# Kernel tuning notes

Measured on AMD Instinct MI355X. Metric: run time of the kernel, lower is better.

The kernel has to match this reference:

```python
import jax, jax.numpy as jnp
import numpy as np

CUTOFF = 4.0
D_RBF = 20


def _rbf_consts():
    # e3nn soft_one_hot_linspace, basis='gaussian', cutoff=False
    values = np.linspace(0.0, CUTOFF, D_RBF)
    step = values[1] - values[0]
    # RadialBasis normalization buffers: 4000 uniform samples, unbiased std
    rs = np.linspace(0.0, CUTOFF, 4001)[1:]
    bs = np.exp(-(((rs[:, None] - values[None, :]) / step) ** 2)) / 1.12
    mean = bs.mean(0)
    inv_std = 1.0 / bs.std(0, ddof=1)
    return (jnp.asarray(values, jnp.float32), jnp.float32(step),
            jnp.asarray(mean, jnp.float32), jnp.asarray(inv_std, jnp.float32))


def setup_inputs() -> dict:
    N, P, E = 2000, 50000, 300000
    Ds, Dv, H, HO = 256, 128, 256, 128
    din = Ds + Dv + D_RBF + Dv  # 532
    key = jax.random.key(0)
    ks = jax.random.split(key, 12)
    atom_xyz = jax.random.uniform(ks[0], (N, 3), jnp.float32, 0.0, 8.0)
    probe_xyz = jax.random.uniform(ks[1], (P, 3), jnp.float32, 0.0, 8.0)
    cell = jnp.eye(3, dtype=jnp.float32)[None] * 8.0  # [1,3,3]
    src = jax.random.randint(ks[2], (E,), 0, N)
    dst = jax.random.randint(ks[3], (E,), 0, P)
    edges = jnp.stack([src, dst], axis=-1).astype(jnp.int32)  # [E,2]
    edges_displacement = jax.random.randint(ks[4], (E, 3), -1, 2).astype(jnp.float32)
    S_final = jax.random.normal(ks[5], (N, Ds), jnp.float32)
    V_final = jax.random.normal(ks[6], (N, Dv, 3), jnp.float32)
    s = 0.02
    return {
        'atom_xyz': atom_xyz, 'probe_xyz': probe_xyz, 'cell': cell,
        'edges': edges, 'edges_displacement': edges_displacement,
        'S_final': S_final, 'V_final': V_final,
        'ln_gamma': jnp.ones((din,), jnp.float32),
        'ln_beta': jnp.zeros((din,), jnp.float32),
        'W1': jax.random.normal(ks[7], (din, H), jnp.float32) * s,
        'b1': jnp.zeros((H,), jnp.float32),
        'W2': jax.random.normal(ks[8], (H, H), jnp.float32) * s,
        'b2': jnp.zeros((H,), jnp.float32),
        'Wo1': jax.random.normal(ks[9], (H, HO), jnp.float32) * s,
        'bo1': jnp.zeros((HO,), jnp.float32),
        'Wo2': jax.random.normal(ks[10], (HO, 1), jnp.float32) * s,
        'bo2': jnp.full((1,), -10.0, jnp.float32),
    }


def reference(atom_xyz, probe_xyz, cell, edges, edges_displacement,
              S_final, V_final, ln_gamma, ln_beta,
              W1, b1, W2, b2, Wo1, bo1, Wo2, bo2):
    values, step, rbf_mean, rbf_inv_std = _rbf_consts()
    src, dst = edges[:, 0], edges[:, 1]
    # PBC displacement: edges_displacement @ cell (single graph -> cell[0])
    disp = edges_displacement @ cell[0]                     # [E,3]
    vec = probe_xyz[dst] - (atom_xyz[src] + disp)           # [E,3]
    d = jnp.maximum(jnp.linalg.norm(vec, axis=-1, keepdims=True), 1e-8)
    r_hat = vec / d                                         # [E,3]
    ds = d[:, 0]                                            # [E]
    # RBF (gaussian soft one-hot) + normalization
    diff = (ds[:, None] - values) / step
    e = (jnp.exp(-diff * diff) / 1.12 - rbf_mean) * rbf_inv_std  # [E,20]
    x = ds / CUTOFF
    x5 = x ** 5
    env = (1.0 - 21.0 * x5 + 35.0 * x5 * x - 15.0 * x5 * x * x)
    env = env * (ds < CUTOFF).astype(jnp.float32)           # [E]
    # geometric invariants
    q = jnp.einsum('ek,eck->ec', r_hat, V_final[src])       # [E,Dv]
    n_atom = jnp.linalg.norm(V_final, axis=-1)              # [N,Dv]
    feat = jnp.concatenate([S_final[src], n_atom[src], e, q], axis=-1)  # [E,532]
    # LayerNorm
    mu = feat.mean(-1, keepdims=True)
    var = feat.var(-1, keepdims=True)
    feat = (feat - mu) * jax.lax.rsqrt(var + 1e-5) * ln_gamma + ln_beta
    # message MLP
    h = jax.nn.silu(feat @ W1 + b1)
    h = jax.nn.silu(h @ W2 + b2)                            # [E,256]
    # envelope-weighted scatter-add to probes
    m_p = jax.ops.segment_sum(h * env[:, None], dst,
                              num_segments=probe_xyz.shape[0])  # [P,256]
    # output MLP
    o = jax.nn.silu(m_p @ Wo1 + bo1)
    rho = o @ Wo2 + bo2                                     # [P,1]
    return rho[:, 0]
```

## Files before the change

### kernel.cpp

```cpp
#include <hip/hip_runtime.h>
#include <hip/hip_bf16.h>
#include <hip/hip_fp16.h>

#define DIN 532
#define DRBF 20
#define EB 32

typedef __attribute__((ext_vector_type(8))) short s8v;
typedef __attribute__((ext_vector_type(4))) float f4v;

static __device__ __forceinline__ float silu_f(float x){
    return x * __builtin_amdgcn_rcpf(1.0f + __expf(-x));
}
static __device__ __forceinline__ short f2bf(float x){
    __hip_bfloat16 b = __float2bfloat16(x);
    return *(short*)&b;
}
static __device__ __forceinline__ s8v pack8(float4 f0, float4 f1){
    s8v r;
    r[0]=f2bf(f0.x); r[1]=f2bf(f0.y); r[2]=f2bf(f0.z); r[3]=f2bf(f0.w);
    r[4]=f2bf(f1.x); r[5]=f2bf(f1.y); r[6]=f2bf(f1.z); r[7]=f2bf(f1.w);
    return r;
}
static __device__ __forceinline__ s8v pack8p(const float* p){
    float4 f0 = *(const float4*)p, f1 = *(const float4*)(p + 4);
    return pack8(f0, f1);
}
static __device__ __forceinline__ bool detect_bf16(const void* cellraw){
    float c0 = ((const float*)cellraw)[0];
    return !(c0 > 7.5f && c0 < 8.5f);
}
static __device__ __forceinline__ float loadr(const void* p, bool isbf, long idx){
    if (isbf) return __bfloat162float(((const __hip_bfloat16*)p)[idx]);
    return ((const float*)p)[idx];
}

struct ConvArgs {
    const void* src[10];
    float*      dst[10];
    int         sz[10];
    int         total;
};

__global__ __launch_bounds__(256) void k_pre(ConvArgs ca,
    const void* W1r, const void* gammar, const void* betar, const void* b1r,
    const void* W2r, const void* Wo1r, const void* cellraw,
    float* Gpart, float* Bpart, float* rbfc,
    short* w1ef, short* w2f, short* w1f, short* wo1f)
{
    int b = blockIdx.x, t = threadIdx.x;
    bool isbf = detect_bf16(cellraw);
    if (b < 256){
        int stride = 256 * 256;
        for (int i = b*256 + t; i < ca.total; i += stride){
            int idx = i, k = 0;
            while (idx >= ca.sz[k]) { idx -= ca.sz[k]; k++; }
            float v = 0.0f;
            if (ca.src[k]) v = loadr(ca.src[k], isbf, idx);
            ca.dst[k][idx] = v;
        }
        return;
    }
    int pb = b - 256;
    if (pb < 17){
        int i0 = pb * 32, i1 = min(i0 + 32, DIN);
        float g = 0.0f, bb = 0.0f;
        for (int i = i0; i < i1; i++){
            float w  = loadr(W1r, isbf, (long)i*256 + t);
            g  += loadr(gammar, isbf, i) * w;
            bb += loadr(betar,  isbf, i) * w;
        }
        if (pb == 0) bb += loadr(b1r, isbf, t);
        Gpart[pb*256 + t] = g;
        Bpart[pb*256 + t] = bb;
        return;
    }
    if (pb == 17){
        __shared__ float ssum[DRBF][8], ssq[DRBF][8];
        if (t < 160){
            int m = t >> 3, c = t & 7;
            const float step = 4.0f/19.0f;
            float vm = step * m;
            float s = 0.0f, ss = 0.0f;
            for (int i = c*500 + 1; i <= c*500 + 500; i++){
                float r = 0.001f * (float)i;
                float u = (r - vm) / step;
                float bv = __expf(-u*u) * (1.0f/1.12f);
                s += bv; ss += bv*bv;
            }
            ssum[m][c] = s; ssq[m][c] = ss;
        }
        __syncthreads();
        if (t < DRBF){
            float s = 0.0f, ss = 0.0f;
            for (int c = 0; c < 8; c++){ s += ssum[t][c]; ss += ssq[t][c]; }
            float mean = s / 4000.0f;
            float var  = (ss - s*s/4000.0f) / 3999.0f;
            rbfc[t]        = mean;
            rbfc[DRBF + t] = rsqrtf(var);
        }
        return;
    }
    int wid = t >> 6, lane = t & 63;
    int q8 = (lane >> 4) * 8, nl = lane & 15;
    if (pb <= 21){
        int f = (pb - 18)*4 + wid;
        for (int j = 0; j < 8; j++){
            int kk = q8 + j;
            int n  = f*16 + nl;
            float v = (kk < DRBF)
                ? loadr(gammar, isbf, 384 + kk) * loadr(W1r, isbf, (long)(384 + kk)*256 + n)
                : 0.0f;
            w1ef[((f << 6) | lane)*8 + j] = f2bf(v);
        }
    } else if (pb <= 53){
        int f = (pb - 22)*4 + wid;
        int ks = f & 7;
        for (int j = 0; j < 8; j++){
            int kk = ks*32 + q8 + j;
            int n  = (f >> 3)*16 + nl;
            w2f[((f << 6) | lane)*8 + j] = f2bf(loadr(W2r, isbf, (long)kk*256 + n));
        }
    } else if (pb <= 117){
        int f = (pb - 54)*4 + wid;
        int ksg = f >> 4, ntg = f & 15;
        int base;
        if (ksg < 8)       base = ksg * 32;
        else if (ksg < 12) base = 256 + (ksg - 8) * 32;
        else               base = 404 + (ksg - 12) * 32;
        for (int j = 0; j < 8; j++){
            int kk = base + q8 + j;
            int n  = ntg*16 + nl;
            w1f[((f << 6) | lane)*8 + j] =
                f2bf(loadr(gammar, isbf, kk) * loadr(W1r, isbf, (long)kk*256 + n));
        }
    } else {
        int f = (pb - 118)*4 + wid;
        int ks = f & 7;
        for (int j = 0; j < 8; j++){
            int kk = ks*32 + q8 + j;
            int n  = (f >> 3)*16 + nl;
            wo1f[((f << 6) | lane)*8 + j] = f2bf(loadr(Wo1r, isbf, (long)kk*128 + n));
        }
    }
}

__global__ __launch_bounds__(1024) void k_mid(
    const float* S, const float* V, const short* w1f, float4* AM,
    float* scal, int N,
    const int* edges, const void* edraw, const float* cell,
    const float* axyz, const float* pxyz,
    int* etot, int* flag, int2* esd, float4* geo, float* m_p,
    const void* cellraw, int E,
    const float* Gpart, const float* Bpart, float* Gv, float* Bb,
    int GA, int GG)
{
    int b = blockIdx.x, t = threadIdx.x;
    int wid = t >> 6, lane = t & 63;

    if (b < GA){
        __shared__ float Sl[16][260];
        __shared__ float Vxl[16][132], Vyl[16][132], Vzl[16][132], nll[16][132];
        int q = lane >> 4, ml = lane & 15;
        int a0 = b * 16;

        #pragma unroll
        for (int rep = 0; rep < 4; rep++){
            int i = rep*1024 + t;
            int a = i >> 8, c = i & 255;
            Sl[a][c] = S[(size_t)min(a0 + a, N - 1)*256 + c];
        }
        #pragma unroll
        for (int rep = 0; rep < 2; rep++){
            int i = rep*1024 + t;
            int a = i >> 7, c = i & 127;
            const float* vp = &V[(size_t)min(a0 + a, N - 1)*384 + 3*c];
            float x = vp[0], y = vp[1], z = vp[2];
            Vxl[a][c] = x; Vyl[a][c] = y; Vzl[a][c] = z;
            nll[a][c] = sqrtf(x*x + y*y + z*z);
        }
        __syncthreads();

        {
            float v[11];
            #pragma unroll
            for (int k = 0; k < 11; k++) v[k] = 0.0f;
            #pragma unroll
            for (int e0 = 0; e0 < 256; e0 += 64){
                float s = Sl[wid][e0 + lane];
                v[0] += s; v[1] += s*s;
            }
            #pragma unroll
            for (int e0 = 0; e0 < 128; e0 += 64){
                int e = e0 + lane;
                float n = nll[wid][e], x = Vxl[wid][e], y = Vyl[wid][e], z = Vzl[wid][e];
                v[0] += n;   v[1] += n*n;
                v[2] += x;   v[3] += y;   v[4] += z;
                v[5] += x*x; v[6] += x*y; v[7] += x*z;
                v[8] += y*y; v[9] += y*z; v[10] += z*z;
            }
            #pragma unroll
            for (int k = 0; k < 11; k++)
                for (int off2 = 32; off2 > 0; off2 >>= 1)
                    v[k] += __shfl_xor(v[k], off2, 64);
            if (lane == 0 && a0 + wid < N)
                for (int k = 0; k < 11; k++) scal[(a0 + wid)*12 + k] = v[k];
        }

        f4v zz = {0.0f, 0.0f, 0.0f, 0.0f};
        f4v aA1 = zz, aM0 = zz, aM1 = zz, aM2 = zz;

        #pragma unroll
        for (int ks = 0; ks < 8; ks++){
            s8v av = pack8p(&Sl[ml][ks*32 + q*8]);
            s8v bf = ((const s8v*)w1f)[(((ks << 4) | wid) << 6) | lane];
            aA1 = __builtin_amdgcn_mfma_f32_16x16x32_bf16(av, bf, aA1, 0, 0, 0);
        }
        #pragma unroll
        for (int ks = 0; ks < 4; ks++){
            s8v av = pack8p(&nll[ml][ks*32 + q*8]);
            s8v bf = ((const s8v*)w1f)[((((8 + ks) << 4) | wid) << 6) | lane];
            aA1 = __builtin_amdgcn_mfma_f32_16x16x32_bf16(av, bf, aA1, 0, 0, 0);
        }
        #pragma unroll
        for (int ks = 0; ks < 4; ks++){
            s8v ax = pack8p(&Vxl[ml][ks*32 + q*8]);
            s8v ay = pack8p(&Vyl[ml][ks*32 + q*8]);
            s8v az = pack8p(&Vzl[ml][ks*32 + q*8]);
            s8v bf = ((const s8v*)w1f)[((((12 + ks) << 4) | wid) << 6) | lane];
            aM0 = __builtin_amdgcn_mfma_f32_16x16x32_bf16(ax, bf, aM0, 0, 0, 0);
            aM1 = __builtin_amdgcn_mfma_f32_16x16x32_bf16(ay, bf, aM1, 0, 0, 0);
            aM2 = __builtin_amdgcn_mfma_f32_16x16x32_bf16(az, bf, aM2, 0, 0, 0);
        }

        #pragma unroll
        for (int reg = 0; reg < 4; reg++){
            int atom = a0 + (q << 2) + reg;
            if (atom < N)
                AM[(size_t)atom*256 + ((wid << 4) | ml)] =
                    make_float4(aA1[reg], aM0[reg], aM1[reg], aM2[reg]);
        }
        return;
    }

    if (b < GA + GG){
        __shared__ int wcnt[16], wbase[16];
        bool isbf = detect_bf16(cellraw);
        float c0=cell[0],c1=cell[1],c2=cell[2],c3=cell[3],c4=cell[4];
        float c5=cell[5],c6=cell[6],c7=cell[7],c8=cell[8];
        int i = (b - GA)*1024 + t;

        bool act = false;
        int s = 0, dd = 0;
        float r0 = 0.f, r1 = 0.f, r2 = 0.f, dn = 0.f;
        if (i < E){
            s = edges[2*i]; dd = edges[2*i + 1];
            float d0 = loadr(edraw, isbf, 3L*i);
            float d1 = loadr(edraw, isbf, 3L*i + 1);
            float d2 = loadr(edraw, isbf, 3L*i + 2);
            float dx = d0*c0 + d1*c3 + d2*c6;
            float dy = d0*c1 + d1*c4 + d2*c7;
            float dz = d0*c2 + d1*c5 + d2*c8;
            float vx = pxyz[3*dd]   - (axyz[3*s]   + dx);
            float vy = pxyz[3*dd+1] - (axyz[3*s+1] + dy);
            float vz = pxyz[3*dd+2] - (axyz[3*s+2] + dz);
            dn = fmaxf(sqrtf(vx*vx + vy*vy + vz*vz), 1e-8f);
            act = dn < 4.0f;
            float inv = __builtin_amdgcn_rcpf(dn);
            r0 = vx*inv; r1 = vy*inv; r2 = vz*inv;
        }
        unsigned long long mask = __ballot(act);
        if (lane == 0) wcnt[wid] = __popcll(mask);
        __syncthreads();
        if (t == 0){
            int tot = 0;
            #pragma unroll
            for (int w2 = 0; w2 < 16; w2++) tot += wcnt[w2];
            int base = tot ? atomicAdd(etot, tot) : 0;
            int run = base;
            #pragma unroll
            for (int w2 = 0; w2 < 16; w2++){ wbase[w2] = run; run += wcnt[w2]; }
        }
        __syncthreads();
        if (act){
            int pos = wbase[wid] + __popcll(mask & ((1ULL << lane) - 1ULL));
            esd[pos] = make_int2(s, dd);
            geo[pos] = make_float4(r0, r1, r2, dn);
            if (atomicExch(&flag[dd], 1) == 0){
                float4 z = make_float4(0.f, 0.f, 0.f, 0.f);
                float4* p = (float4*)&m_p[(size_t)dd*256];
                #pragma unroll 4
                for (int k = 0; k < 64; k++) p[k] = z;
            }
        }
        return;
    }

    if (t < 256){
        float g = 0.0f, bb = 0.0f;
        #pragma unroll
        for (int i = 0; i < 17; i++){
            g  += Gpart[i*256 + t];
            bb += Bpart[i*256 + t];
        }
        Gv[t] = g;
        Bb[t] = bb;
    }
}

__global__ __launch_bounds__(256, 2) void k_edge(
    const int2* esd, const float4* geo, const int* etot, const float* scal,
    const float4* AM, const float* Gv, const float* Bb, const float* b2,
    const short* w1ef, const short* w2f, const float* rbfc, float* m_p)
{
    __shared__ float Gl[256], Bbl[256], b2l[256];
    __shared__ float rmean[DRBF], rinv[DRBF];
    __shared__ int   esrc[EB], edst[EB];
    __shared__ float rh0[EB], rh1[EB], rh2[EB], envv[EB], muv[EB], av[EB];
    __shared__ __align__(16) short ebfl[EB][32];
    __shared__ __align__(16) short afrag[2][8][64][8];

    int t = threadIdx.x, wid = t >> 6, lane = t & 63;
    int q = lane >> 4, ml_ = lane & 15;
    Gl[t] = Gv[t]; Bbl[t] = Bb[t]; b2l[t] = b2[t];
    if (t < DRBF){ rmean[t] = rbfc[t]; rinv[t] = rbfc[DRBF + t]; }
    __syncthreads();

    int Ea = etot[0];
    int ntiles = (Ea + EB - 1) / EB;

    for (int tile = blockIdx.x; tile < ntiles; tile += gridDim.x){
        if (t < EB){
            int epos = tile*EB + t;
            if (epos < Ea){
                int2 sd = esd[epos];
                float4 g = geo[epos];
                float r0 = g.x, r1 = g.y, r2 = g.z, dn = g.w;
                float x = dn * 0.25f;
                float x2 = x*x, x4 = x2*x2, x5 = x4*x;
                float env = 1.0f - 21.0f*x5 + 35.0f*x5*x - 15.0f*x5*x2;
                const float step = 4.0f/19.0f;
                float se = 0.0f, sse = 0.0f;
                for (int m = 0; m < DRBF; m++){
                    float u  = (dn - step*m) / step;
                    float bv = __expf(-u*u) * (1.0f/1.12f);
                    float em = (bv - rmean[m]) * rinv[m];
                    ebfl[t][m] = f2bf(em);
                    se += em; sse += em*em;
                }
                for (int m = DRBF; m < 32; m++) ebfl[t][m] = 0;
                const float* sc = &scal[sd.x*12];
                float sumq = r0*sc[2] + r1*sc[3] + r2*sc[4];
                float ssqq = r0*r0*sc[5] + r1*r1*sc[8] + r2*r2*sc[10]
                           + 2.0f*(r0*r1*sc[6] + r0*r2*sc[7] + r1*r2*sc[9]);
                float mu  = (sc[0] + se + sumq) * (1.0f/(float)DIN);
                float msq = (sc[1] + sse + ssqq) * (1.0f/(float)DIN);
                float a   = rsqrtf(fmaxf(msq - mu*mu, 0.0f) + 1e-5f);
                esrc[t] = sd.x; edst[t] = sd.y;
                rh0[t] = r0; rh1[t] = r1; rh2[t] = r2;
                envv[t] = env; muv[t] = mu; av[t] = a;
            } else {
                esrc[t] = 0; edst[t] = 0;
                rh0[t] = rh1[t] = rh2[t] = 0.0f;
                envv[t] = 0.0f; muv[t] = 0.0f; av[t] = 0.0f;
                for (int m = 0; m < 32; m++) ebfl[t][m] = 0;
            }
        }
        __syncthreads();

        f4v zz = {0.0f, 0.0f, 0.0f, 0.0f};
        f4v az[2][4];
        s8v ea0 = *(const s8v*)&ebfl[ml_][q*8];
        s8v ea1 = *(const s8v*)&ebfl[16 + ml_][q*8];
        #pragma unroll
        for (int nt = 0; nt < 4; nt++){
            s8v bw = ((const s8v*)w1ef)[(((wid << 2) | nt) << 6) | lane];
            az[0][nt] = __builtin_amdgcn_mfma_f32_16x16x32_bf16(ea0, bw, zz, 0, 0, 0);
            az[1][nt] = __builtin_amdgcn_mfma_f32_16x16x32_bf16(ea1, bw, zz, 0, 0, 0);
        }

        float gk[4], bbk[4];
        #pragma unroll
        for (int nt = 0; nt < 4; nt++){
            int k = (wid << 6) | (nt << 4) | ml_;
            gk[nt] = Gl[k]; bbk[nt] = Bbl[k];
        }
        #pragma unroll
        for (int mt = 0; mt < 2; mt++){
            #pragma unroll
            for (int reg = 0; reg < 4; reg++){
                int e_ = (mt << 4) | (q << 2) | reg;
                int s_ = esrc[e_];
                float r0 = rh0[e_], r1 = rh1[e_], r2 = rh2[e_];
                float mu = muv[e_], a_ = av[e_];
                const float4* AMr = &AM[(size_t)s_*256 + ((wid << 6) | ml_)];
                #pragma unroll
                for (int nt = 0; nt < 4; nt++){
                    float4 am = AMr[nt << 4];
                    float z = az[mt][nt][reg] + am.x + r0*am.y + r1*am.z + r2*am.w;
                    float y = a_*(z - mu*gk[nt]) + bbk[nt];
                    float h1 = silu_f(y);
                    int ks = (wid << 1) | (nt >> 1);
                    int col = ((nt & 1) << 4) | ml_;
                    int lanep = ((col >> 3) << 4) | (q << 2) | reg;
                    afrag[mt][ks][lanep][col & 7] = f2bf(h1);
                }
            }
        }
        __syncthreads();

        f4v acc[2][4];
        #pragma unroll
        for (int mt = 0; mt < 2; mt++)
            #pragma unroll
            for (int nt = 0; nt < 4; nt++) acc[mt][nt] = zz;
        #pragma unroll
        for (int ks = 0; ks < 8; ks++){
            s8v a0 = *(const s8v*)&afrag[0][ks][lane][0];
            s8v a1 = *(const s8v*)&afrag[1][ks][lane][0];
            #pragma unroll
            for (int nt = 0; nt < 4; nt++){
                s8v bf = ((const s8v*)w2f)[(((((wid << 2) | nt) << 3) | ks) << 6) | lane];
                acc[0][nt] = __builtin_amdgcn_mfma_f32_16x16x32_bf16(a0, bf, acc[0][nt], 0, 0, 0);
                acc[1][nt] = __builtin_amdgcn_mfma_f32_16x16x32_bf16(a1, bf, acc[1][nt], 0, 0, 0);
            }
        }

        float b2k[4];
        #pragma unroll
        for (int nt = 0; nt < 4; nt++) b2k[nt] = b2l[(wid << 6) | (nt << 4) | ml_];
        #pragma unroll
        for (int mt = 0; mt < 2; mt++){
            #pragma unroll
            for (int reg = 0; reg < 4; reg++){
                int e_ = (mt << 4) | (q << 2) | reg;
                float env = envv[e_];
                if (env != 0.0f){
                    int dd = edst[e_];
                    float* mrow = &m_p[(size_t)dd*256 + (wid << 6) + ml_];
                    #pragma unroll
                    for (int nt = 0; nt < 4; nt++){
                        float z2 = acc[mt][nt][reg] + b2k[nt];
                        atomicAdd(&mrow[nt << 4], silu_f(z2) * env);
                    }
                }
            }
        }
        __syncthreads();
    }
}

__global__ __launch_bounds__(256) void k_probe(
    const float* m_p, const int* flag, const short* wo1f, const float* bo1,
    const float* Wo2, const float* bo2, void* out, const void* cellraw, int P)
{
    int t = threadIdx.x, wid = t >> 6, lane = t & 63;
    int q = lane >> 4, ml = lane & 15;
    int p0 = blockIdx.x * 128 + wid * 32;
    const float4* mp4 = (const float4*)m_p;

    f4v zz = {0.0f, 0.0f, 0.0f, 0.0f};
    f4v acc[2][8];
    #pragma unroll
    for (int mt = 0; mt < 2; mt++)
        #pragma unroll
        for (int nt = 0; nt < 8; nt++) acc[mt][nt] = zz;

    int row0 = min(p0 + ml, P - 1);
    int row1 = min(p0 + 16 + ml, P - 1);
    bool f0 = flag[row0] != 0;
    bool f1 = flag[row1] != 0;
    s8v zero8 = {0,0,0,0,0,0,0,0};

    #pragma unroll
    for (int ks = 0; ks < 8; ks++){
        int c = ks*8 + q*2;
        s8v a0 = zero8, a1 = zero8;
        if (f0){
            float4 f00 = mp4[(size_t)row0*64 + c], f01 = mp4[(size_t)row0*64 + c + 1];
            a0 = pack8(f00, f01);
        }
        if (f1){
            float4 f10 = mp4[(size_t)row1*64 + c], f11 = mp4[(size_t)row1*64 + c + 1];
            a1 = pack8(f10, f11);
        }
        #pragma unroll
        for (int nt = 0; nt < 8; nt++){
            s8v bf = ((const s8v*)wo1f)[(((nt << 3) | ks) << 6) | lane];
            acc[0][nt] = __builtin_amdgcn_mfma_f32_16x16x32_bf16(a0, bf, acc[0][nt], 0, 0, 0);
            acc[1][nt] = __builtin_amdgcn_mfma_f32_16x16x32_bf16(a1, bf, acc[1][nt], 0, 0, 0);
        }
    }

    float bo1v[8], wo2v[8];
    #pragma unroll
    for (int nt = 0; nt < 8; nt++){
        int n = (nt << 4) | ml;
        bo1v[nt] = bo1[n];
        wo2v[nt] = Wo2[n];
    }
    bool isbf = detect_bf16(cellraw);
    float bo2v = bo2[0];

    #pragma unroll
    for (int mt = 0; mt < 2; mt++){
        #pragma unroll
        for (int reg = 0; reg < 4; reg++){
            float s = 0.0f;
            #pragma unroll
            for (int nt = 0; nt < 8; nt++)
                s += silu_f(acc[mt][nt][reg] + bo1v[nt]) * wo2v[nt];
            s += __shfl_xor(s, 1, 64);
            s += __shfl_xor(s, 2, 64);
            s += __shfl_xor(s, 4, 64);
            s += __shfl_xor(s, 8, 64);
            if (ml == 0){
                int p = p0 + (mt << 4) + (q << 2) + reg;
                if (p < P){
                    float rho = s + bo2v;
                    if (isbf) ((__hip_bfloat16*)out)[p] = __float2bfloat16(rho);
                    else      ((float*)out)[p] = rho;
                }
            }
        }
    }
}

extern "C" void kernel_launch(void* const* d_in, const int* in_sizes, int n_in,
                              void* d_out, int out_size, void* d_ws, size_t ws_size,
                              hipStream_t stream)
{
    const int N = in_sizes[0] / 3;
    const int P = in_sizes[1] / 3;
    const int E = in_sizes[3] / 2;

    float* w = (float*)d_ws;
    size_t off = 0;
    auto carve = [&](size_t n) -> float* {
        float* p = w + off;
        off += (n + 63) & ~(size_t)63;
        return p;
    };

    const int conv_din[9] = {6, 5, 1, 0, 12, 14, 15, 2, 16};
    float* cdst[9];
    int    csz[9];
    int total = 0;
    for (int k = 0; k < 9; k++){
        csz[k]  = in_sizes[conv_din[k]];
        cdst[k] = carve(csz[k]);
        total  += csz[k];
    }
    float* c_V     = cdst[0];
    float* c_S     = cdst[1];
    float* c_probe = cdst[2];
    float* c_atom  = cdst[3];
    float* c_b2    = cdst[4];
    float* c_bo1   = cdst[5];
    float* c_Wo2   = cdst[6];
    float* c_cell  = cdst[7];
    float* c_bo2   = cdst[8];

    float* rbfc  = carve(2 * DRBF);
    float* AMf   = carve((size_t)N * 256 * 4);
    float* scal  = carve((size_t)N * 12);
    float* w1ef  = carve(16 * 64 * 8 / 2);
    float* w2f   = carve(128 * 64 * 8 / 2);
    float* w1f   = carve(256 * 64 * 8 / 2);
    float* wo1f  = carve(64 * 64 * 8 / 2);
    float* m_p   = carve((size_t)P * 256);
    int*   etot  = (int*)carve(64);
    int*   flag  = (int*)carve(P);
    float* Gv    = carve(256);
    float* Bb    = carve(256);
    float* Gpart = carve(17 * 256);
    float* Bpart = carve(17 * 256);
    int*   esd   = (int*)carve((size_t)E * 2);
    float* geo   = carve((size_t)E * 4);

    ConvArgs ca;
    for (int k = 0; k < 9; k++){
        ca.src[k] = d_in[conv_din[k]];
        ca.dst[k] = cdst[k];
        ca.sz[k]  = csz[k];
    }
    ca.src[9] = nullptr;
    ca.dst[9] = (float*)etot;
    ca.sz[9]  = 64 + P;
    ca.total  = total + 64 + P;

    const int* d_edges = (const int*)d_in[3];
    const int GA = (N + 15) / 16;
    const int GG = (E + 1023) / 1024;

    k_pre<<<390, 256, 0, stream>>>(ca,
        d_in[9], d_in[7], d_in[8], d_in[10], d_in[11], d_in[13], d_in[2],
        Gpart, Bpart, rbfc,
        (short*)w1ef, (short*)w2f, (short*)w1f, (short*)wo1f);
    k_mid<<<GA + GG + 1, 1024, 0, stream>>>(
        c_S, c_V, (const short*)w1f, (float4*)AMf, scal, N,
        d_edges, d_in[4], c_cell, c_atom, c_probe,
        etot, flag, (int2*)esd, (float4*)geo, m_p, d_in[2], E,
        Gpart, Bpart, Gv, Bb, GA, GG);
    k_edge<<<512, 256, 0, stream>>>(
        (const int2*)esd, (const float4*)geo, etot, scal,
        (const float4*)AMf, Gv, Bb, c_b2,
        (const short*)w1ef, (const short*)w2f, rbfc, m_p);
    k_probe<<<(P + 127) / 128, 256, 0, stream>>>(
        m_p, flag, (const short*)wo1f, c_bo1, c_Wo2, c_bo2, d_out, d_in[2], P);
}
```

Measured before the change: 177.6 us.

## Merge four kernels into one cooperative persistent kernel with grid syncs

```diff
diff --git a/kernel.cpp b/kernel.cpp
--- a/kernel.cpp
+++ b/kernel.cpp
@@ -1,6 +1,8 @@
 #include <hip/hip_runtime.h>
 #include <hip/hip_bf16.h>
-#include <hip/hip_fp16.h>
+#include <hip/hip_cooperative_groups.h>
+
+namespace cg = cooperative_groups;
 
 #define DIN 532
 #define DRBF 20
@@ -35,491 +37,479 @@
     return ((const float*)p)[idx];
 }
 
-struct ConvArgs {
-    const void* src[10];
-    float*      dst[10];
-    int         sz[10];
-    int         total;
+struct AtomSmem {
+    float Sl[16][260];
+    float Vx[16][132], Vy[16][132], Vz[16][132], nl[16][132];
 };
-
-__global__ __launch_bounds__(256) void k_pre(ConvArgs ca,
-    const void* W1r, const void* gammar, const void* betar, const void* b1r,
-    const void* W2r, const void* Wo1r, const void* cellraw,
-    float* Gpart, float* Bpart, float* rbfc,
-    short* w1ef, short* w2f, short* w1f, short* wo1f)
+struct EdgeSmem {
+    short afrag[2][8][64][8];
+    short ebfl[EB][32];
+    float Gl[256], Bbl[256], b2l[256];
+    float rmean[32], rinv[32];
+    int   esrc[EB], edst[EB];
+    float rh0[EB], rh1[EB], rh2[EB], envv[EB], muv[EB], av[EB];
+};
+struct GeomSmem { int wcnt[4], wbase[4]; };
+struct RbfSmem  { float ssum[DRBF][8], ssq[DRBF][8]; };
+
+struct KArgs {
+    const void* csrc[10]; float* cdst[10]; int csz[10]; int ctotal;
+    const void *W1r, *gammar, *betar, *b1r, *W2r, *Wo1r, *cellraw, *edraw;
+    const int* edges;
+    float *Gpart, *Bpart, *Gv, *Bb, *rbfc;
+    short *w1ef, *w2f, *w1f, *wo1f;
+    float* scal; float4* AM;
+    int *etot, *flag; int2* esd; float4* geo; float* m_p;
+    const float *c_S, *c_V, *c_probe, *c_atom, *c_b2, *c_bo1, *c_Wo2, *c_cell, *c_bo2;
+    void* out;
+    int N, P, E, NAT;
+};
+
+__global__ __launch_bounds__(256, 3) void k_all(KArgs a)
 {
-    int b = blockIdx.x, t = threadIdx.x;
-    bool isbf = detect_bf16(cellraw);
-    if (b < 256){
-        int stride = 256 * 256;
-        for (int i = b*256 + t; i < ca.total; i += stride){
-            int idx = i, k = 0;
-            while (idx >= ca.sz[k]) { idx -= ca.sz[k]; k++; }
-            float v = 0.0f;
-            if (ca.src[k]) v = loadr(ca.src[k], isbf, idx);
-            ca.dst[k][idx] = v;
+    cg::grid_group gridg = cg::this_grid();
+    __shared__ __align__(16) char smem[sizeof(AtomSmem)];
+    const int G = gridDim.x, bid = blockIdx.x, t = threadIdx.x;
+    const int wid = t >> 6, lane = t & 63;
+    const int q = lane >> 4, ml = lane & 15;
+    const bool isbf = detect_bf16(a.cellraw);
+    const f4v zz = {0.0f, 0.0f, 0.0f, 0.0f};
+
+    for (int i = bid*256 + t; i < a.ctotal; i += G*256){
+        int idx = i, k = 0;
+        while (idx >= a.csz[k]){ idx -= a.csz[k]; k++; }
+        float v = 0.0f;
+        if (a.csrc[k]) v = loadr(a.csrc[k], isbf, idx);
+        a.cdst[k][idx] = v;
+    }
+    for (int j = bid; j < 134; j += G){
+        if (j < 17){
+            int i0 = j * 32, i1 = min(i0 + 32, DIN);
+            float g = 0.0f, bb = 0.0f;
+            for (int i = i0; i < i1; i++){
+                float w  = loadr(a.W1r, isbf, (long)i*256 + t);
+                g  += loadr(a.gammar, isbf, i) * w;
+                bb += loadr(a.betar,  isbf, i) * w;
+            }
+            if (j == 0) bb += loadr(a.b1r, isbf, t);
+            a.Gpart[j*256 + t] = g;
+            a.Bpart[j*256 + t] = bb;
+        } else if (j == 17){
+            RbfSmem* rs = (RbfSmem*)smem;
+            if (t < 160){
+                int m = t >> 3, c = t & 7;
+                const float step = 4.0f/19.0f;
+                float vm = step * m;
+                float s = 0.0f, ss = 0.0f;
+                for (int i = c*500 + 1; i <= c*500 + 500; i++){
+                    float r = 0.001f * (float)i;
+                    float u = (r - vm) / step;
+                    float bv = __expf(-u*u) * (1.0f/1.12f);
+                    s += bv; ss += bv*bv;
+                }
+                rs->ssum[m][c] = s; rs->ssq[m][c] = ss;
+            }
+            __syncthreads();
+            if (t < DRBF){
+                float s = 0.0f, ss = 0.0f;
+                for (int c = 0; c < 8; c++){ s += rs->ssum[t][c]; ss += rs->ssq[t][c]; }
+                float mean = s / 4000.0f;
+                float var  = (ss - s*s/4000.0f) / 3999.0f;
+                a.rbfc[t]        = mean;
+                a.rbfc[DRBF + t] = rsqrtf(var);
+            }
+            __syncthreads();
+        } else {
+            int q8 = (lane >> 4) * 8, nl_ = lane & 15;
+            if (j <= 21){
+                int f = (j - 18)*4 + wid;
+                for (int jj = 0; jj < 8; jj++){
+                    int kk = q8 + jj;
+                    int n  = f*16 + nl_;
+                    float v = (kk < DRBF)
+                        ? loadr(a.gammar, isbf, 384 + kk) * loadr(a.W1r, isbf, (long)(384 + kk)*256 + n)
+                        : 0.0f;
+                    a.w1ef[((f << 6) | lane)*8 + jj] = f2bf(v);
+                }
+            } else if (j <= 53){
+                int f = (j - 22)*4 + wid;
+                int ks = f & 7;
+                for (int jj = 0; jj < 8; jj++){
+                    int kk = ks*32 + q8 + jj;
+                    int n  = (f >> 3)*16 + nl_;
+                    a.w2f[((f << 6) | lane)*8 + jj] = f2bf(loadr(a.W2r, isbf, (long)kk*256 + n));
+                }
+            } else if (j <= 117){
+                int f = (j - 54)*4 + wid;
+                int ksg = f >> 4, ntg = f & 15;
+                int base;
+                if (ksg < 8)       base = ksg * 32;
+                else if (ksg < 12) base = 256 + (ksg - 8) * 32;
+                else               base = 404 + (ksg - 12) * 32;
+                for (int jj = 0; jj < 8; jj++){
+                    int kk = base + q8 + jj;
+                    int n  = ntg*16 + nl_;
+                    a.w1f[((f << 6) | lane)*8 + jj] =
+                        f2bf(loadr(a.gammar, isbf, kk) * loadr(a.W1r, isbf, (long)kk*256 + n));
+                }
+            } else {
+                int f = (j - 118)*4 + wid;
+                int ks = f & 7;
+                for (int jj = 0; jj < 8; jj++){
+                    int kk = ks*32 + q8 + jj;
+                    int n  = (f >> 3)*16 + nl_;
+                    a.wo1f[((f << 6) | lane)*8 + jj] = f2bf(loadr(a.Wo1r, isbf, (long)kk*128 + n));
+                }
+            }
         }
-        return;
-    }
-    int pb = b - 256;
-    if (pb < 17){
-        int i0 = pb * 32, i1 = min(i0 + 32, DIN);
-        float g = 0.0f, bb = 0.0f;
-        for (int i = i0; i < i1; i++){
-            float w  = loadr(W1r, isbf, (long)i*256 + t);
-            g  += loadr(gammar, isbf, i) * w;
-            bb += loadr(betar,  isbf, i) * w;
+    }
+    __threadfence();
+    gridg.sync();
+
+    AtomSmem* as = (AtomSmem*)smem;
+    const int NJ1 = a.NAT*5 + 1;
+    for (int j = bid; j < NJ1; j += G){
+        if (j < a.NAT){
+            for (int a2 = 0; a2 < 4; a2++){
+                int atom = j*16 + wid*4 + a2;
+                int row = min(atom, a.N - 1);
+                float v[11];
+                #pragma unroll
+                for (int k = 0; k < 11; k++) v[k] = 0.0f;
+                for (int e = lane; e < 256; e += 64){
+                    float s = a.c_S[(size_t)row*256 + e];
+                    v[0] += s; v[1] += s*s;
+                }
+                for (int e = lane; e < 128; e += 64){
+                    const float* vp = &a.c_V[(size_t)row*384 + 3*e];
+                    float x = vp[0], y = vp[1], z = vp[2];
+                    float n = sqrtf(x*x + y*y + z*z);
+                    v[0] += n;   v[1] += n*n;
+                    v[2] += x;   v[3] += y;   v[4] += z;
+                    v[5] += x*x; v[6] += x*y; v[7] += x*z;
+                    v[8] += y*y; v[9] += y*z; v[10] += z*z;
+                }
+                #pragma unroll
+                for (int k = 0; k < 11; k++)
+                    for (int off2 = 32; off2 > 0; off2 >>= 1)
+                        v[k] += __shfl_xor(v[k], off2, 64);
+                if (lane == 0 && atom < a.N)
+                    for (int k = 0; k < 11; k++) a.scal[atom*12 + k] = v[k];
+            }
+        } else if (j < a.NAT*5){
+            int g = j - a.NAT;
+            int at = g >> 2, ng = g & 3;
+            __syncthreads();
+            #pragma unroll
+            for (int rep = 0; rep < 16; rep++){
+                int i = rep*256 + t;
+                int aa = i >> 8, c = i & 255;
+                as->Sl[aa][c] = a.c_S[(size_t)min(at*16 + aa, a.N - 1)*256 + c];
+            }
+            #pragma unroll
+            for (int rep = 0; rep < 8; rep++){
+                int i = rep*256 + t;
+                int aa = i >> 7, c = i & 127;
+                const float* vp = &a.c_V[(size_t)min(at*16 + aa, a.N - 1)*384 + 3*c];
+                float x = vp[0], y = vp[1], z = vp[2];
+                as->Vx[aa][c] = x; as->Vy[aa][c] = y; as->Vz[aa][c] = z;
+                as->nl[aa][c] = sqrtf(x*x + y*y + z*z);
+            }
+            __syncthreads();
+            int ntg = ng*4 + wid;
+            f4v aA1 = zz, aM0 = zz, aM1 = zz, aM2 = zz;
+            #pragma unroll
+            for (int ks = 0; ks < 8; ks++){
+                s8v av = pack8p(&as->Sl[ml][ks*32 + q*8]);
+                s8v bf = ((const s8v*)a.w1f)[(((ks << 4) | ntg) << 6) | lane];
+                aA1 = __builtin_amdgcn_mfma_f32_16x16x32_bf16(av, bf, aA1, 0, 0, 0);
+            }
+            #pragma unroll
+            for (int ks = 0; ks < 4; ks++){
+                s8v av = pack8p(&as->nl[ml][ks*32 + q*8]);
+                s8v bf = ((const s8v*)a.w1f)[((((8 + ks) << 4) | ntg) << 6) | lane];
+                aA1 = __builtin_amdgcn_mfma_f32_16x16x32_bf16(av, bf, aA1, 0, 0, 0);
+            }
+            #pragma unroll
+            for (int ks = 0; ks < 4; ks++){
+                s8v ax = pack8p(&as->Vx[ml][ks*32 + q*8]);
+                s8v ay = pack8p(&as->Vy[ml][ks*32 + q*8]);
+                s8v az = pack8p(&as->Vz[ml][ks*32 + q*8]);
+                s8v bf = ((const s8v*)a.w1f)[((((12 + ks) << 4) | ntg) << 6) | lane];
+                aM0 = __builtin_amdgcn_mfma_f32_16x16x32_bf16(ax, bf, aM0, 0, 0, 0);
+                aM1 = __builtin_amdgcn_mfma_f32_16x16x32_bf16(ay, bf, aM1, 0, 0, 0);
+                aM2 = __builtin_amdgcn_mfma_f32_16x16x32_bf16(az, bf, aM2, 0, 0, 0);
+            }
+            #pragma unroll
+            for (int reg = 0; reg < 4; reg++){
+                int atom = at*16 + (q << 2) + reg;
+                if (atom < a.N)
+                    a.AM[(size_t)atom*256 + ((ntg << 4) | ml)] =
+                        make_float4(aA1[reg], aM0[reg], aM1[reg], aM2[reg]);
+            }
+            __syncthreads();
+        } else {
+            float g2 = 0.0f, bb = 0.0f;
+            #pragma unroll
+            for (int i = 0; i < 17; i++){
+                g2 += a.Gpart[i*256 + t];
+                bb += a.Bpart[i*256 + t];
+            }
+            a.Gv[t] = g2;
+            a.Bb[t] = bb;
         }
-        if (pb == 0) bb += loadr(b1r, isbf, t);
-        Gpart[pb*256 + t] = g;
-        Bpart[pb*256 + t] = bb;
-        return;
-    }
-    if (pb == 17){
-        __shared__ float ssum[DRBF][8], ssq[DRBF][8];
-        if (t < 160){
-            int m = t >> 3, c = t & 7;
-            const float step = 4.0f/19.0f;
-            float vm = step * m;
-            float s = 0.0f, ss = 0.0f;
-            for (int i = c*500 + 1; i <= c*500 + 500; i++){
-                float r = 0.001f * (float)i;
-                float u = (r - vm) / step;
-                float bv = __expf(-u*u) * (1.0f/1.12f);
-                s += bv; ss += bv*bv;
-            }
-            ssum[m][c] = s; ssq[m][c] = ss;
+    }
+    __syncthreads();
+    {
+        GeomSmem* gs = (GeomSmem*)smem;
+        float c0 = a.c_cell[0], c1 = a.c_cell[1], c2 = a.c_cell[2];
+        float c3 = a.c_cell[3], c4 = a.c_cell[4], c5 = a.c_cell[5];
+        float c6 = a.c_cell[6], c7 = a.c_cell[7], c8 = a.c_cell[8];
+        for (long base = (long)bid*256; base < a.E; base += (long)G*256){
+            int i = (int)base + t;
+            bool in = i < a.E;
+            bool act = false;
+            int s = 0, dd = 0;
+            float r0 = 0.f, r1 = 0.f, r2 = 0.f, dn = 0.f;
+            if (in){
+                s = a.edges[2*i]; dd = a.edges[2*i + 1];
+                float d0 = loadr(a.edraw, isbf, 3L*i);
+                float d1 = loadr(a.edraw, isbf, 3L*i + 1);
+                float d2 = loadr(a.edraw, isbf, 3L*i + 2);
+                float dx = d0*c0 + d1*c3 + d2*c6;
+                float dy = d0*c1 + d1*c4 + d2*c7;
+                float dz = d0*c2 + d1*c5 + d2*c8;
+                float vx = a.c_probe[3*dd]   - (a.c_atom[3*s]   + dx);
+                float vy = a.c_probe[3*dd+1] - (a.c_atom[3*s+1] + dy);
+                float vz = a.c_probe[3*dd+2] - (a.c_atom[3*s+2] + dz);
+                dn = fmaxf(sqrtf(vx*vx + vy*vy + vz*vz), 1e-8f);
+                act = dn < 4.0f;
+                float inv = __builtin_amdgcn_rcpf(dn);
+                r0 = vx*inv; r1 = vy*inv; r2 = vz*inv;
+            }
+            unsigned long long mask = __ballot(act);
+            if (lane == 0) gs->wcnt[wid] = __popcll(mask);
+            __syncthreads();
+            if (t == 0){
+                int tot = gs->wcnt[0] + gs->wcnt[1] + gs->wcnt[2] + gs->wcnt[3];
+                int bse = tot ? atomicAdd(a.etot, tot) : 0;
+                int run = bse;
+                #pragma unroll
+                for (int w2 = 0; w2 < 4; w2++){ gs->wbase[w2] = run; run += gs->wcnt[w2]; }
+            }
+            __syncthreads();
+            if (act){
+                int pos = gs->wbase[wid] + __popcll(mask & ((1ULL << lane) - 1ULL));
+                a.esd[pos] = make_int2(s, dd);
+                a.geo[pos] = make_float4(r0, r1, r2, dn);
+                if (atomicExch(&a.flag[dd], 1) == 0){
+                    float4 z = make_float4(0.f, 0.f, 0.f, 0.f);
+                    float4* p = (float4*)&a.m_p[(size_t)dd*256];
+                    #pragma unroll 4
+                    for (int k = 0; k < 64; k++) p[k] = z;
+                }
+            }
+            __syncthreads();
         }
+    }
+    __threadfence();
+    gridg.sync();
+
+    {
+        EdgeSmem* es = (EdgeSmem*)smem;
+        es->Gl[t] = a.Gv[t]; es->Bbl[t] = a.Bb[t]; es->b2l[t] = a.c_b2[t];
+        if (t < DRBF){ es->rmean[t] = a.rbfc[t]; es->rinv[t] = a.rbfc[DRBF + t]; }
         __syncthreads();
-        if (t < DRBF){
-            float s = 0.0f, ss = 0.0f;
-            for (int c = 0; c < 8; c++){ s += ssum[t][c]; ss += ssq[t][c]; }
-            float mean = s / 4000.0f;
-            float var  = (ss - s*s/4000.0f) / 3999.0f;
-            rbfc[t]        = mean;
-            rbfc[DRBF + t] = rsqrtf(var);
-        }
-        return;
-    }
-    int wid = t >> 6, lane = t & 63;
-    int q8 = (lane >> 4) * 8, nl = lane & 15;
-    if (pb <= 21){
-        int f = (pb - 18)*4 + wid;
-        for (int j = 0; j < 8; j++){
-            int kk = q8 + j;
-            int n  = f*16 + nl;
-            float v = (kk < DRBF)
-                ? loadr(gammar, isbf, 384 + kk) * loadr(W1r, isbf, (long)(384 + kk)*256 + n)
-                : 0.0f;
-            w1ef[((f << 6) | lane)*8 + j] = f2bf(v);
-        }
-    } else if (pb <= 53){
-        int f = (pb - 22)*4 + wid;
-        int ks = f & 7;
-        for (int j = 0; j < 8; j++){
-            int kk = ks*32 + q8 + j;
-            int n  = (f >> 3)*16 + nl;
-            w2f[((f << 6) | lane)*8 + j] = f2bf(loadr(W2r, isbf, (long)kk*256 + n));
-        }
-    } else if (pb <= 117){
-        int f = (pb - 54)*4 + wid;
-        int ksg = f >> 4, ntg = f & 15;
-        int base;
-        if (ksg < 8)       base = ksg * 32;
-        else if (ksg < 12) base = 256 + (ksg - 8) * 32;
-        else               base = 404 + (ksg - 12) * 32;
-        for (int j = 0; j < 8; j++){
-            int kk = base + q8 + j;
-            int n  = ntg*16 + nl;
-            w1f[((f << 6) | lane)*8 + j] =
-                f2bf(loadr(gammar, isbf, kk) * loadr(W1r, isbf, (long)kk*256 + n));
-        }
-    } else {
-        int f = (pb - 118)*4 + wid;
-        int ks = f & 7;
-        for (int j = 0; j < 8; j++){
-            int kk = ks*32 + q8 + j;
-            int n  = (f >> 3)*16 + nl;
-            wo1f[((f << 6) | lane)*8 + j] = f2bf(loadr(Wo1r, isbf, (long)kk*128 + n));
-        }
-    }
-}
-
-__global__ __launch_bounds__(1024) void k_mid(
-    const float* S, const float* V, const short* w1f, float4* AM,
-    float* scal, int N,
-    const int* edges, const void* edraw, const float* cell,
-    const float* axyz, const float* pxyz,
-    int* etot, int* flag, int2* esd, float4* geo, float* m_p,
-    const void* cellraw, int E,
-    const float* Gpart, const float* Bpart, float* Gv, float* Bb,
-    int GA, int GG)
-{
-    int b = blockIdx.x, t = threadIdx.x;
-    int wid = t >> 6, lane = t & 63;
-
-    if (b < GA){
-        __shared__ float Sl[16][260];
-        __shared__ float Vxl[16][132], Vyl[16][132], Vzl[16][132], nll[16][132];
-        int q = lane >> 4, ml = lane & 15;
-        int a0 = b * 16;
-
-        #pragma unroll
-        for (int rep = 0; rep < 4; rep++){
-            int i = rep*1024 + t;
-            int a = i >> 8, c = i & 255;
-            Sl[a][c] = S[(size_t)min(a0 + a, N - 1)*256 + c];
-        }
-        #pragma unroll
-        for (int rep = 0; rep < 2; rep++){
-            int i = rep*1024 + t;
-            int a = i >> 7, c = i & 127;
-            const float* vp = &V[(size_t)min(a0 + a, N - 1)*384 + 3*c];
-            float x = vp[0], y = vp[1], z = vp[2];
-            Vxl[a][c] = x; Vyl[a][c] = y; Vzl[a][c] = z;
-            nll[a][c] = sqrtf(x*x + y*y + z*z);
-        }
-        __syncthreads();
-
-        {
-            float v[11];
-            #pragma unroll
-            for (int k = 0; k < 11; k++) v[k] = 0.0f;
-            #pragma unroll
-            for (int e0 = 0; e0 < 256; e0 += 64){
-                float s = Sl[wid][e0 + lane];
-                v[0] += s; v[1] += s*s;
-            }
-            #pragma unroll
-            for (int e0 = 0; e0 < 128; e0 += 64){
-                int e = e0 + lane;
-                float n = nll[wid][e], x = Vxl[wid][e], y = Vyl[wid][e], z = Vzl[wid][e];
-                v[0] += n;   v[1] += n*n;
-                v[2] += x;   v[3] += y;   v[4] += z;
-                v[5] += x*x; v[6] += x*y; v[7] += x*z;
-                v[8] += y*y; v[9] += y*z; v[10] += z*z;
-            }
-            #pragma unroll
-            for (int k = 0; k < 11; k++)
-                for (int off2 = 32; off2 > 0; off2 >>= 1)
-                    v[k] += __shfl_xor(v[k], off2, 64);
-            if (lane == 0 && a0 + wid < N)
-                for (int k = 0; k < 11; k++) scal[(a0 + wid)*12 + k] = v[k];
-        }
-
-        f4v zz = {0.0f, 0.0f, 0.0f, 0.0f};
-        f4v aA1 = zz, aM0 = zz, aM1 = zz, aM2 = zz;
-
-        #pragma unroll
-        for (int ks = 0; ks < 8; ks++){
-            s8v av = pack8p(&Sl[ml][ks*32 + q*8]);
-            s8v bf = ((const s8v*)w1f)[(((ks << 4) | wid) << 6) | lane];
-            aA1 = __builtin_amdgcn_mfma_f32_16x16x32_bf16(av, bf, aA1, 0, 0, 0);
-        }
-        #pragma unroll
-        for (int ks = 0; ks < 4; ks++){
-            s8v av = pack8p(&nll[ml][ks*32 + q*8]);
-            s8v bf = ((const s8v*)w1f)[((((8 + ks) << 4) | wid) << 6) | lane];
-            aA1 = __builtin_amdgcn_mfma_f32_16x16x32_bf16(av, bf, aA1, 0, 0, 0);
-        }
-        #pragma unroll
-        for (int ks = 0; ks < 4; ks++){
-            s8v ax = pack8p(&Vxl[ml][ks*32 + q*8]);
-            s8v ay = pack8p(&Vyl[ml][ks*32 + q*8]);
-            s8v az = pack8p(&Vzl[ml][ks*32 + q*8]);
-            s8v bf = ((const s8v*)w1f)[((((12 + ks) << 4) | wid) << 6) | lane];
-            aM0 = __builtin_amdgcn_mfma_f32_16x16x32_bf16(ax, bf, aM0, 0, 0, 0);
-            aM1 = __builtin_amdgcn_mfma_f32_16x16x32_bf16(ay, bf, aM1, 0, 0, 0);
-            aM2 = __builtin_amdgcn_mfma_f32_16x16x32_bf16(az, bf, aM2, 0, 0, 0);
-        }
-
-        #pragma unroll
-        for (int reg = 0; reg < 4; reg++){
-            int atom = a0 + (q << 2) + reg;
-            if (atom < N)
-                AM[(size_t)atom*256 + ((wid << 4) | ml)] =
-                    make_float4(aA1[reg], aM0[reg], aM1[reg], aM2[reg]);
-        }
-        return;
-    }
-
-    if (b < GA + GG){
-        __shared__ int wcnt[16], wbase[16];
-        bool isbf = detect_bf16(cellraw);
-        float c0=cell[0],c1=cell[1],c2=cell[2],c3=cell[3],c4=cell[4];
-        float c5=cell[5],c6=cell[6],c7=cell[7],c8=cell[8];
-        int i = (b - GA)*1024 + t;
-
-        bool act = false;
-        int s = 0, dd = 0;
-        float r0 = 0.f, r1 = 0.f, r2 = 0.f, dn = 0.f;
-        if (i < E){
-            s = edges[2*i]; dd = edges[2*i + 1];
-            float d0 = loadr(edraw, isbf, 3L*i);
-            float d1 = loadr(edraw, isbf, 3L*i + 1);
-            float d2 = loadr(edraw, isbf, 3L*i + 2);
-            float dx = d0*c0 + d1*c3 + d2*c6;
-            float dy = d0*c1 + d1*c4 + d2*c7;
-            float dz = d0*c2 + d1*c5 + d2*c8;
-            float vx = pxyz[3*dd]   - (axyz[3*s]   + dx);
-            float vy = pxyz[3*dd+1] - (axyz[3*s+1] + dy);
-            float vz = pxyz[3*dd+2] - (axyz[3*s+2] + dz);
-            dn = fmaxf(sqrtf(vx*vx + vy*vy + vz*vz), 1e-8f);
-            act = dn < 4.0f;
-            float inv = __builtin_amdgcn_rcpf(dn);
-            r0 = vx*inv; r1 = vy*inv; r2 = vz*inv;
-        }
-        unsigned long long mask = __ballot(act);
-        if (lane == 0) wcnt[wid] = __popcll(mask);
-        __syncthreads();
-        if (t == 0){
-            int tot = 0;
-            #pragma unroll
-            for (int w2 = 0; w2 < 16; w2++) tot += wcnt[w2];
-            int base = tot ? atomicAdd(etot, tot) : 0;
-            int run = base;
-            #pragma unroll
-            for (int w2 = 0; w2 < 16; w2++){ wbase[w2] = run; run += wcnt[w2]; }
-        }
-        __syncthreads();
-        if (act){
-            int pos = wbase[wid] + __popcll(mask & ((1ULL << lane) - 1ULL));
-            esd[pos] = make_int2(s, dd);
-            geo[pos] = make_float4(r0, r1, r2, dn);
-            if (atomicExch(&flag[dd], 1) == 0){
-                float4 z = make_float4(0.f, 0.f, 0.f, 0.f);
-                float4* p = (float4*)&m_p[(size_t)dd*256];
-                #pragma unroll 4
-                for (int k = 0; k < 64; k++) p[k] = z;
-            }
-        }
-        return;
-    }
-
-    if (t < 256){
-        float g = 0.0f, bb = 0.0f;
-        #pragma unroll
-        for (int i = 0; i < 17; i++){
-            g  += Gpart[i*256 + t];
-            bb += Bpart[i*256 + t];
-        }
-        Gv[t] = g;
-        Bb[t] = bb;
-    }
-}
-
-__global__ __launch_bounds__(256, 2) void k_edge(
-    const int2* esd, const float4* geo, const int* etot, const float* scal,
-    const float4* AM, const float* Gv, const float* Bb, const float* b2,
-    const short* w1ef, const short* w2f, const float* rbfc, float* m_p)
-{
-    __shared__ float Gl[256], Bbl[256], b2l[256];
-    __shared__ float rmean[DRBF], rinv[DRBF];
-    __shared__ int   esrc[EB], edst[EB];
-    __shared__ float rh0[EB], rh1[EB], rh2[EB], envv[EB], muv[EB], av[EB];
-    __shared__ __align__(16) short ebfl[EB][32];
-    __shared__ __align__(16) short afrag[2][8][64][8];
-
-    int t = threadIdx.x, wid = t >> 6, lane = t & 63;
-    int q = lane >> 4, ml_ = lane & 15;
-    Gl[t] = Gv[t]; Bbl[t] = Bb[t]; b2l[t] = b2[t];
-    if (t < DRBF){ rmean[t] = rbfc[t]; rinv[t] = rbfc[DRBF + t]; }
-    __syncthreads();
-
-    int Ea = etot[0];
-    int ntiles = (Ea + EB - 1) / EB;
-
-    for (int tile = blockIdx.x; tile < ntiles; tile += gridDim.x){
-        if (t < EB){
-            int epos = tile*EB + t;
-            if (epos < Ea){
-                int2 sd = esd[epos];
-                float4 g = geo[epos];
-                float r0 = g.x, r1 = g.y, r2 = g.z, dn = g.w;
-                float x = dn * 0.25f;
-                float x2 = x*x, x4 = x2*x2, x5 = x4*x;
-                float env = 1.0f - 21.0f*x5 + 35.0f*x5*x - 15.0f*x5*x2;
-                const float step = 4.0f/19.0f;
-                float se = 0.0f, sse = 0.0f;
-                for (int m = 0; m < DRBF; m++){
-                    float u  = (dn - step*m) / step;
-                    float bv = __expf(-u*u) * (1.0f/1.12f);
-                    float em = (bv - rmean[m]) * rinv[m];
-                    ebfl[t][m] = f2bf(em);
-                    se += em; sse += em*em;
-                }
-                for (int m = DRBF; m < 32; m++) ebfl[t][m] = 0;
-                const float* sc = &scal[sd.x*12];
-                float sumq = r0*sc[2] + r1*sc[3] + r2*sc[4];
-                float ssqq = r0*r0*sc[5] + r1*r1*sc[8] + r2*r2*sc[10]
-                           + 2.0f*(r0*r1*sc[6] + r0*r2*sc[7] + r1*r2*sc[9]);
-                float mu  = (sc[0] + se + sumq) * (1.0f/(float)DIN);
-                float msq = (sc[1] + sse + ssqq) * (1.0f/(float)DIN);
-                float a   = rsqrtf(fmaxf(msq - mu*mu, 0.0f) + 1e-5f);
-                esrc[t] = sd.x; edst[t] = sd.y;
-                rh0[t] = r0; rh1[t] = r1; rh2[t] = r2;
-                envv[t] = env; muv[t] = mu; av[t] = a;
-            } else {
-                esrc[t] = 0; edst[t] = 0;
-                rh0[t] = rh1[t] = rh2[t] = 0.0f;
-                envv[t] = 0.0f; muv[t] = 0.0f; av[t] = 0.0f;
-                for (int m = 0; m < 32; m++) ebfl[t][m] = 0;
-            }
-        }
-        __syncthreads();
-
-        f4v zz = {0.0f, 0.0f, 0.0f, 0.0f};
-        f4v az[2][4];
-        s8v ea0 = *(const s8v*)&ebfl[ml_][q*8];
-        s8v ea1 = *(const s8v*)&ebfl[16 + ml_][q*8];
-        #pragma unroll
-        for (int nt = 0; nt < 4; nt++){
-            s8v bw = ((const s8v*)w1ef)[(((wid << 2) | nt) << 6) | lane];
-            az[0][nt] = __builtin_amdgcn_mfma_f32_16x16x32_bf16(ea0, bw, zz, 0, 0, 0);
-            az[1][nt] = __builtin_amdgcn_mfma_f32_16x16x32_bf16(ea1, bw, zz, 0, 0, 0);
-        }
-
-        float gk[4], bbk[4];
-        #pragma unroll
-        for (int nt = 0; nt < 4; nt++){
-            int k = (wid << 6) | (nt << 4) | ml_;
-            gk[nt] = Gl[k]; bbk[nt] = Bbl[k];
-        }
-        #pragma unroll
-        for (int mt = 0; mt < 2; mt++){
-            #pragma unroll
-            for (int reg = 0; reg < 4; reg++){
-                int e_ = (mt << 4) | (q << 2) | reg;
-                int s_ = esrc[e_];
-                float r0 = rh0[e_], r1 = rh1[e_], r2 = rh2[e_];
-                float mu = muv[e_], a_ = av[e_];
-                const float4* AMr = &AM[(size_t)s_*256 + ((wid << 6) | ml_)];
-                #pragma unroll
-                for (int nt = 0; nt < 4; nt++){
-                    float4 am = AMr[nt << 4];
-                    float z = az[mt][nt][reg] + am.x + r0*am.y + r1*am.z + r2*am.w;
-                    float y = a_*(z - mu*gk[nt]) + bbk[nt];
-                    float h1 = silu_f(y);
-                    int ks = (wid << 1) | (nt >> 1);
-                    int col = ((nt & 1) << 4) | ml_;
-                    int lanep = ((col >> 3) << 4) | (q << 2) | reg;
-                    afrag[mt][ks][lanep][col & 7] = f2bf(h1);
-                }
-            }
-        }
-        __syncthreads();
-
-        f4v acc[2][4];
-        #pragma unroll
-        for (int mt = 0; mt < 2; mt++)
-            #pragma unroll
-            for (int nt = 0; nt < 4; nt++) acc[mt][nt] = zz;
-        #pragma unroll
-        for (int ks = 0; ks < 8; ks++){
-            s8v a0 = *(const s8v*)&afrag[0][ks][lane][0];
-            s8v a1 = *(const s8v*)&afrag[1][ks][lane][0];
+        int Ea = a.etot[0];
+        int ntiles = (Ea + EB - 1) / EB;
+        for (int tile = bid; tile < ntiles; tile += G){
+            if (t < EB){
+                int epos = tile*EB + t;
+                if (epos < Ea){
+                    int2 sd = a.esd[epos];
+                    float4 g = a.geo[epos];
+                    float r0 = g.x, r1 = g.y, r2 = g.z, dn = g.w;
+                    float x = dn * 0.25f;
+                    float x2 = x*x, x4 = x2*x2, x5 = x4*x;
+                    float env = 1.0f - 21.0f*x5 + 35.0f*x5*x - 15.0f*x5*x2;
+                    const float step = 4.0f/19.0f;
+                    float se = 0.0f, sse = 0.0f;
+                    for (int m = 0; m < DRBF; m++){
+                        float u  = (dn - step*m) / step;
+                        float bv = __expf(-u*u) * (1.0f/1.12f);
+                        float em = (bv - es->rmean[m]) * es->rinv[m];
+                        es->ebfl[t][m] = f2bf(em);
+                        se += em; sse += em*em;
+                    }
+                    for (int m = DRBF; m < 32; m++) es->ebfl[t][m] = 0;
+                    const float* sc = &a.scal[sd.x*12];
+                    float sumq = r0*sc[2] + r1*sc[3] + r2*sc[4];
+                    float ssqq = r0*r0*sc[5] + r1*r1*sc[8] + r2*r2*sc[10]
+                               + 2.0f*(r0*r1*sc[6] + r0*r2*sc[7] + r1*r2*sc[9]);
+                    float mu  = (sc[0] + se + sumq) * (1.0f/(float)DIN);
+                    float msq = (sc[1] + sse + ssqq) * (1.0f/(float)DIN);
+                    float aa  = rsqrtf(fmaxf(msq - mu*mu, 0.0f) + 1e-5f);
+                    es->esrc[t] = sd.x; es->edst[t] = sd.y;
+                    es->rh0[t] = r0; es->rh1[t] = r1; es->rh2[t] = r2;
+                    es->envv[t] = env; es->muv[t] = mu; es->av[t] = aa;
+                } else {
+                    es->esrc[t] = 0; es->edst[t] = 0;
+                    es->rh0[t] = es->rh1[t] = es->rh2[t] = 0.0f;
+                    es->envv[t] = 0.0f; es->muv[t] = 0.0f; es->av[t] = 0.0f;
+                    for (int m = 0; m < 32; m++) es->ebfl[t][m] = 0;
+                }
+            }
+            __syncthreads();
+
+            f4v az2[2][4];
+            s8v ea0 = *(const s8v*)&es->ebfl[ml][q*8];
+            s8v ea1 = *(const s8v*)&es->ebfl[16 + ml][q*8];
             #pragma unroll
             for (int nt = 0; nt < 4; nt++){
-                s8v bf = ((const s8v*)w2f)[(((((wid << 2) | nt) << 3) | ks) << 6) | lane];
-                acc[0][nt] = __builtin_amdgcn_mfma_f32_16x16x32_bf16(a0, bf, acc[0][nt], 0, 0, 0);
-                acc[1][nt] = __builtin_amdgcn_mfma_f32_16x16x32_bf16(a1, bf, acc[1][nt], 0, 0, 0);
-            }
-        }
-
-        float b2k[4];
-        #pragma unroll
-        for (int nt = 0; nt < 4; nt++) b2k[nt] = b2l[(wid << 6) | (nt << 4) | ml_];
-        #pragma unroll
-        for (int mt = 0; mt < 2; mt++){
-            #pragma unroll
-            for (int reg = 0; reg < 4; reg++){
-                int e_ = (mt << 4) | (q << 2) | reg;
-                float env = envv[e_];
-                if (env != 0.0f){
-                    int dd = edst[e_];
-                    float* mrow = &m_p[(size_t)dd*256 + (wid << 6) + ml_];
+                s8v bw = ((const s8v*)a.w1ef)[(((wid << 2) | nt) << 6) | lane];
+                az2[0][nt] = __builtin_amdgcn_mfma_f32_16x16x32_bf16(ea0, bw, zz, 0, 0, 0);
+                az2[1][nt] = __builtin_amdgcn_mfma_f32_16x16x32_bf16(ea1, bw, zz, 0, 0, 0);
+            }
+
+            float gk[4], bbk[4];
+            #pragma unroll
+            for (int nt = 0; nt < 4; nt++){
+                int k = (wid << 6) | (nt << 4) | ml;
+                gk[nt] = es->Gl[k]; bbk[nt] = es->Bbl[k];
+            }
+            #pragma unroll
+            for (int mt = 0; mt < 2; mt++){
+                #pragma unroll
+                for (int reg = 0; reg < 4; reg++){
+                    int e_ = (mt << 4) | (q << 2) | reg;
+                    int s_ = es->esrc[e_];
+                    float r0 = es->rh0[e_], r1 = es->rh1[e_], r2 = es->rh2[e_];
+                    float mu = es->muv[e_], a_ = es->av[e_];
+                    const float4* AMr = &a.AM[(size_t)s_*256 + ((wid << 6) | ml)];
                     #pragma unroll
                     for (int nt = 0; nt < 4; nt++){
-                        float z2 = acc[mt][nt][reg] + b2k[nt];
-                        atomicAdd(&mrow[nt << 4], silu_f(z2) * env);
+                        float4 am = AMr[nt << 4];
+                        float z = az2[mt][nt][reg] + am.x + r0*am.y + r1*am.z + r2*am.w;
+                        float y = a_*(z - mu*gk[nt]) + bbk[nt];
+                        float h1 = silu_f(y);
+                        int ks = (wid << 1) | (nt >> 1);
+                        int col = ((nt & 1) << 4) | ml;
+                        int lanep = ((col >> 3) << 4) | (q << 2) | reg;
+                        es->afrag[mt][ks][lanep][col & 7] = f2bf(h1);
                     }
                 }
             }
+            __syncthreads();
+
+            f4v acc[2][4];
+            #pragma unroll
+            for (int mt = 0; mt < 2; mt++)
+                #pragma unroll
+                for (int nt = 0; nt < 4; nt++) acc[mt][nt] = zz;
+            #pragma unroll
+            for (int ks = 0; ks < 8; ks++){
+                s8v a0 = *(const s8v*)&es->afrag[0][ks][lane][0];
+                s8v a1 = *(const s8v*)&es->afrag[1][ks][lane][0];
+                #pragma unroll
+                for (int nt = 0; nt < 4; nt++){
+                    s8v bf = ((const s8v*)a.w2f)[(((((wid << 2) | nt) << 3) | ks) << 6) | lane];
+                    acc[0][nt] = __builtin_amdgcn_mfma_f32_16x16x32_bf16(a0, bf, acc[0][nt], 0, 0, 0);
+                    acc[1][nt] = __builtin_amdgcn_mfma_f32_16x16x32_bf16(a1, bf, acc[1][nt], 0, 0, 0);
+                }
+            }
+
+            float b2k[4];
+            #pragma unroll
+            for (int nt = 0; nt < 4; nt++) b2k[nt] = es->b2l[(wid << 6) | (nt << 4) | ml];
+            #pragma unroll
+            for (int mt = 0; mt < 2; mt++){
+                #pragma unroll
+                for (int reg = 0; reg < 4; reg++){
+                    int e_ = (mt << 4) | (q << 2) | reg;
+                    float env = es->envv[e_];
+                    if (env != 0.0f){
+                        int dd = es->edst[e_];
+                        float* mrow = &a.m_p[(size_t)dd*256 + (wid << 6) + ml];
+                        #pragma unroll
+                        for (int nt = 0; nt < 4; nt++){
+                            float z2 = acc[mt][nt][reg] + b2k[nt];
+                            atomicAdd(&mrow[nt << 4], silu_f(z2) * env);
+                        }
+                    }
+                }
+            }
+            __syncthreads();
         }
-        __syncthreads();
-    }
-}
-
-__global__ __launch_bounds__(256) void k_probe(
-    const float* m_p, const int* flag, const short* wo1f, const float* bo1,
-    const float* Wo2, const float* bo2, void* out, const void* cellraw, int P)
-{
-    int t = threadIdx.x, wid = t >> 6, lane = t & 63;
-    int q = lane >> 4, ml = lane & 15;
-    int p0 = blockIdx.x * 128 + wid * 32;
-    const float4* mp4 = (const float4*)m_p;
-
-    f4v zz = {0.0f, 0.0f, 0.0f, 0.0f};
-    f4v acc[2][8];
-    #pragma unroll
-    for (int mt = 0; mt < 2; mt++)
-        #pragma unroll
-        for (int nt = 0; nt < 8; nt++) acc[mt][nt] = zz;
-
-    int row0 = min(p0 + ml, P - 1);
-    int row1 = min(p0 + 16 + ml, P - 1);
-    bool f0 = flag[row0] != 0;
-    bool f1 = flag[row1] != 0;
-    s8v zero8 = {0,0,0,0,0,0,0,0};
-
-    #pragma unroll
-    for (int ks = 0; ks < 8; ks++){
-        int c = ks*8 + q*2;
-        s8v a0 = zero8, a1 = zero8;
-        if (f0){
-            float4 f00 = mp4[(size_t)row0*64 + c], f01 = mp4[(size_t)row0*64 + c + 1];
-            a0 = pack8(f00, f01);
-        }
-        if (f1){
-            float4 f10 = mp4[(size_t)row1*64 + c], f11 = mp4[(size_t)row1*64 + c + 1];
-            a1 = pack8(f10, f11);
-        }
-        #pragma unroll
-        for (int nt = 0; nt < 8; nt++){
-            s8v bf = ((const s8v*)wo1f)[(((nt << 3) | ks) << 6) | lane];
-            acc[0][nt] = __builtin_amdgcn_mfma_f32_16x16x32_bf16(a0, bf, acc[0][nt], 0, 0, 0);
-            acc[1][nt] = __builtin_amdgcn_mfma_f32_16x16x32_bf16(a1, bf, acc[1][nt], 0, 0, 0);
-        }
-    }
-
-    float bo1v[8], wo2v[8];
-    #pragma unroll
-    for (int nt = 0; nt < 8; nt++){
-        int n = (nt << 4) | ml;
-        bo1v[nt] = bo1[n];
-        wo2v[nt] = Wo2[n];
-    }
-    bool isbf = detect_bf16(cellraw);
-    float bo2v = bo2[0];
-
-    #pragma unroll
-    for (int mt = 0; mt < 2; mt++){
-        #pragma unroll
-        for (int reg = 0; reg < 4; reg++){
-            float s = 0.0f;
-            #pragma unroll
-            for (int nt = 0; nt < 8; nt++)
-                s += silu_f(acc[mt][nt][reg] + bo1v[nt]) * wo2v[nt];
-            s += __shfl_xor(s, 1, 64);
-            s += __shfl_xor(s, 2, 64);
-            s += __shfl_xor(s, 4, 64);
-            s += __shfl_xor(s, 8, 64);
-            if (ml == 0){
-                int p = p0 + (mt << 4) + (q << 2) + reg;
-                if (p < P){
-                    float rho = s + bo2v;
-                    if (isbf) ((__hip_bfloat16*)out)[p] = __float2bfloat16(rho);
-                    else      ((float*)out)[p] = rho;
+    }
+    __threadfence();
+    gridg.sync();
+
+    {
+        const float4* mp4 = (const float4*)a.m_p;
+        int ptiles = (a.P + 127) / 128;
+        for (int j = bid; j < ptiles; j += G){
+            int p0 = j*128 + wid*32;
+            f4v acc[2][8];
+            #pragma unroll
+            for (int mt = 0; mt < 2; mt++)
+                #pragma unroll
+                for (int nt = 0; nt < 8; nt++) acc[mt][nt] = zz;
+
+            int row0 = min(p0 + ml, a.P - 1);
+            int row1 = min(p0 + 16 + ml, a.P - 1);
+            bool f0 = a.flag[row0] != 0;
+            bool f1 = a.flag[row1] != 0;
+            s8v zero8 = {0,0,0,0,0,0,0,0};
+
+            #pragma unroll
+            for (int ks = 0; ks < 8; ks++){
+                int c = ks*8 + q*2;
+                s8v a0 = zero8, a1 = zero8;
+                if (f0){
+                    float4 f00 = mp4[(size_t)row0*64 + c], f01 = mp4[(size_t)row0*64 + c + 1];
+                    a0 = pack8(f00, f01);
+                }
+                if (f1){
+                    float4 f10 = mp4[(size_t)row1*64 + c], f11 = mp4[(size_t)row1*64 + c + 1];
+                    a1 = pack8(f10, f11);
+                }
+                #pragma unroll
+                for (int nt = 0; nt < 8; nt++){
+                    s8v bf = ((const s8v*)a.wo1f)[(((nt << 3) | ks) << 6) | lane];
+                    acc[0][nt] = __builtin_amdgcn_mfma_f32_16x16x32_bf16(a0, bf, acc[0][nt], 0, 0, 0);
+                    acc[1][nt] = __builtin_amdgcn_mfma_f32_16x16x32_bf16(a1, bf, acc[1][nt], 0, 0, 0);
+                }
+            }
+
+            float bo1v[8], wo2v[8];
+            #pragma unroll
+            for (int nt = 0; nt < 8; nt++){
+                int n = (nt << 4) | ml;
+                bo1v[nt] = a.c_bo1[n];
+                wo2v[nt] = a.c_Wo2[n];
+            }
+            float bo2v = a.c_bo2[0];
+
+            #pragma unroll
+            for (int mt = 0; mt < 2; mt++){
+                #pragma unroll
+                for (int reg = 0; reg < 4; reg++){
+                    float s = 0.0f;
+                    #pragma unroll
+                    for (int nt = 0; nt < 8; nt++)
+                        s += silu_f(acc[mt][nt][reg] + bo1v[nt]) * wo2v[nt];
+                    s += __shfl_xor(s, 1, 64);
+                    s += __shfl_xor(s, 2, 64);
+                    s += __shfl_xor(s, 4, 64);
+                    s += __shfl_xor(s, 8, 64);
+                    if (ml == 0){
+                        int p = p0 + (mt << 4) + (q << 2) + reg;
+                        if (p < a.P){
+                            float rho = s + bo2v;
+                            if (isbf) ((__hip_bfloat16*)a.out)[p] = __float2bfloat16(rho);
+                            else      ((float*)a.out)[p] = rho;
+                        }
+                    }
                 }
             }
         }
@@ -551,15 +541,6 @@
         cdst[k] = carve(csz[k]);
         total  += csz[k];
     }
-    float* c_V     = cdst[0];
-    float* c_S     = cdst[1];
-    float* c_probe = cdst[2];
-    float* c_atom  = cdst[3];
-    float* c_b2    = cdst[4];
-    float* c_bo1   = cdst[5];
-    float* c_Wo2   = cdst[6];
-    float* c_cell  = cdst[7];
-    float* c_bo2   = cdst[8];
 
     float* rbfc  = carve(2 * DRBF);
     float* AMf   = carve((size_t)N * 256 * 4);
@@ -578,34 +559,39 @@
     int*   esd   = (int*)carve((size_t)E * 2);
     float* geo   = carve((size_t)E * 4);
 
-    ConvArgs ca;
+    KArgs a;
     for (int k = 0; k < 9; k++){
-        ca.src[k] = d_in[conv_din[k]];
-        ca.dst[k] = cdst[k];
-        ca.sz[k]  = csz[k];
-    }
-    ca.src[9] = nullptr;
-    ca.dst[9] = (float*)etot;
-    ca.sz[9]  = 64 + P;
-    ca.total  = total + 64 + P;
-
-    const int* d_edges = (const int*)d_in[3];
-    const int GA = (N + 15) / 16;
-    const int GG = (E + 1023) / 1024;
-
-    k_pre<<<390, 256, 0, stream>>>(ca,
-        d_in[9], d_in[7], d_in[8], d_in[10], d_in[11], d_in[13], d_in[2],
-        Gpart, Bpart, rbfc,
-        (short*)w1ef, (short*)w2f, (short*)w1f, (short*)wo1f);
-    k_mid<<<GA + GG + 1, 1024, 0, stream>>>(
-        c_S, c_V, (const short*)w1f, (float4*)AMf, scal, N,
-        d_edges, d_in[4], c_cell, c_atom, c_probe,
-        etot, flag, (int2*)esd, (float4*)geo, m_p, d_in[2], E,
-        Gpart, Bpart, Gv, Bb, GA, GG);
-    k_edge<<<512, 256, 0, stream>>>(
-        (const int2*)esd, (const float4*)geo, etot, scal,
-        (const float4*)AMf, Gv, Bb, c_b2,
-        (const short*)w1ef, (const short*)w2f, rbfc, m_p);
-    k_probe<<<(P + 127) / 128, 256, 0, stream>>>(
-        m_p, flag, (const short*)wo1f, c_bo1, c_Wo2, c_bo2, d_out, d_in[2], P);
-}
+        a.csrc[k] = d_in[conv_din[k]];
+        a.cdst[k] = cdst[k];
+        a.csz[k]  = csz[k];
+    }
+    a.csrc[9] = nullptr;
+    a.cdst[9] = (float*)etot;
+    a.csz[9]  = 64 + P;
+    a.ctotal  = total + 64 + P;
+
+    a.W1r = d_in[9];  a.gammar = d_in[7]; a.betar = d_in[8]; a.b1r = d_in[10];
+    a.W2r = d_in[11]; a.Wo1r = d_in[13];  a.cellraw = d_in[2]; a.edraw = d_in[4];
+    a.edges = (const int*)d_in[3];
+    a.Gpart = Gpart; a.Bpart = Bpart; a.Gv = Gv; a.Bb = Bb; a.rbfc = rbfc;
+    a.w1ef = (short*)w1ef; a.w2f = (short*)w2f; a.w1f = (short*)w1f; a.wo1f = (short*)wo1f;
+    a.scal = scal; a.AM = (float4*)AMf;
+    a.etot = etot; a.flag = flag; a.esd = (int2*)esd; a.geo = (float4*)geo; a.m_p = m_p;
+    a.c_V = cdst[0]; a.c_S = cdst[1]; a.c_probe = cdst[2]; a.c_atom = cdst[3];
+    a.c_b2 = cdst[4]; a.c_bo1 = cdst[5]; a.c_Wo2 = cdst[6]; a.c_cell = cdst[7];
+    a.c_bo2 = cdst[8];
+    a.out = d_out;
+    a.N = N; a.P = P; a.E = E; a.NAT = (N + 15) / 16;
+
+    int maxb = 0;
+    hipOccupancyMaxActiveBlocksPerMultiprocessor(&maxb, k_all, 256, 0);
+    if (maxb < 1) maxb = 1;
+    hipDeviceProp_t prop;
+    int dev = 0;
+    hipGetDevice(&dev);
+    hipGetDeviceProperties(&prop, dev);
+    int grid = maxb * prop.multiProcessorCount;
+    if (grid > 1536) grid = 1536;
+    void* params[] = { (void*)&a };
+    hipLaunchCooperativeKernel(k_all, dim3(grid), dim3(256), params, 0, stream);
+}
```

Measured after the change: 394.9 us. 122% more time.
